# Kernel tuning notes

Measured on AMD Instinct MI355X. Metric: run time of the kernel, lower is better.

## Reference

```python
import jax, jax.numpy as jnp
import numpy as np
from jax.scipy.special import logsumexp

NUM_CLASSES = 2
THRESHOLD = 0.35      # overlap_thresh
NEGPOS_RATIO = 7      # neg_pos
VAR0, VAR1 = 0.1, 0.2  # self.variance


def point_form(p):
    # (cx,cy,w,h) -> (x1,y1,x2,y2)
    return jnp.concatenate([p[:, :2] - p[:, 2:] / 2, p[:, :2] + p[:, 2:] / 2], axis=1)


def jaccard(a, b):
    # a: [T,4] xyxy, b: [P,4] xyxy -> IoU [T,P]
    lt = jnp.maximum(a[:, None, :2], b[None, :, :2])
    rb = jnp.minimum(a[:, None, 2:], b[None, :, 2:])
    wh = jnp.clip(rb - lt, 0.0)
    inter = wh[..., 0] * wh[..., 1]
    area_a = ((a[:, 2] - a[:, 0]) * (a[:, 3] - a[:, 1]))[:, None]
    area_b = ((b[:, 2] - b[:, 0]) * (b[:, 3] - b[:, 1]))[None, :]
    return inter / (area_a + area_b - inter)


def encode(matched, priors):
    # matched xyxy [P,4], priors cxcywh [P,4]
    g_cxcy = ((matched[:, :2] + matched[:, 2:]) / 2 - priors[:, :2]) / (VAR0 * priors[:, 2:])
    g_wh = jnp.log((matched[:, 2:] - matched[:, :2]) / priors[:, 2:]) / VAR1
    return jnp.concatenate([g_cxcy, g_wh], axis=1)


def encode_landm(matched, priors):
    m = matched.reshape(-1, 5, 2)  # [P,5,2]
    g = (m - priors[:, None, :2]) / (VAR0 * priors[:, None, 2:])
    return g.reshape(-1, 10)


def match_one(truths, labels, landms, priors):
    # truths [T,4] xyxy, labels [T], landms [T,10], priors [P,4] cxcywh
    overlaps = jaccard(truths, point_form(priors))  # [T,P]
    best_prior_overlap = overlaps.max(axis=1)       # [T]
    best_prior_idx = overlaps.argmax(axis=1)        # [T]
    valid_gt = best_prior_overlap >= 0.2            # hard-gt filter
    best_truth_overlap = overlaps.max(axis=0)       # [P]
    best_truth_idx = overlaps.argmax(axis=0)        # [P]
    # index_fill_(0, best_prior_idx[valid], 2): IoU <= 1 so scatter-max is exact
    best_truth_overlap = best_truth_overlap.at[best_prior_idx].max(
        jnp.where(valid_gt, 2.0, 0.0))
    best_truth_idx = best_truth_idx.at[best_prior_idx].set(jnp.arange(truths.shape[0]))
    matches = truths[best_truth_idx]                # [P,4]
    conf = jnp.where(best_truth_overlap < THRESHOLD, 0.0, labels[best_truth_idx])
    loc = encode(matches, priors)
    landm = encode_landm(landms[best_truth_idx], priors)
    any_valid = valid_gt.any()                      # early-return branch in torch match()
    loc = jnp.where(any_valid, loc, 0.0)
    conf = jnp.where(any_valid, conf, 0.0)
    landm = jnp.where(any_valid, landm, 0.0)
    return loc, conf.astype(jnp.int32), landm


def smooth_l1(x):
    ax = jnp.abs(x)
    return jnp.where(ax < 1.0, 0.5 * ax * ax, ax - 0.5)


def multibox_loss(loc_data, conf_data, landm_data, priors, targets):
    num_priors = priors.shape[0]
    # torch uses .data (detached) for matching/encoding targets
    truths = jax.lax.stop_gradient(targets[..., :4])
    landms_gt = jax.lax.stop_gradient(targets[..., 4:14])
    labels = jax.lax.stop_gradient(targets[..., 14])
    pri = jax.lax.stop_gradient(priors)
    loc_t, conf_t, landm_t = jax.vmap(match_one, in_axes=(0, 0, 0, None))(
        truths, labels, landms_gt, pri)  # [B,P,4], [B,P], [B,P,10]

    # landmark loss over conf_t > 0
    pos1 = conf_t > 0
    N1 = jnp.maximum(pos1.sum().astype(jnp.float32), 1.0)
    loss_landm = jnp.sum(smooth_l1(landm_data - landm_t) * pos1[..., None])

    # localization loss over conf_t != 0; conf_t[pos] = 1
    pos = conf_t != 0
    conf_t = jnp.where(pos, 1, conf_t)
    loss_l = jnp.sum(smooth_l1(loc_data - loc_t) * pos[..., None])

    # per-prior CE = logsumexp(logits) - logit[target]
    ce = logsumexp(conf_data, axis=-1) - jnp.take_along_axis(
        conf_data, conf_t[..., None], axis=-1)[..., 0]  # [B,P]
    # hard negative mining: zero positives, double-argsort rank trick
    rank_loss = jnp.where(pos, 0.0, ce)
    idx_rank = jnp.argsort(jnp.argsort(-rank_loss, axis=1), axis=1)
    num_pos = pos.sum(axis=1, keepdims=True)
    num_neg = jnp.minimum(NEGPOS_RATIO * num_pos, num_priors - 1)
    neg = idx_rank < num_neg
    loss_c = jnp.sum(jnp.where(pos | neg, ce, 0.0))

    N = jnp.maximum(num_pos.sum().astype(jnp.float32), 1.0)
    return loss_l / N, loss_c / N, loss_landm / N1


def setup_inputs() -> dict:
    key = jax.random.key(0)
    ks = jax.random.split(key, 8)
    B, P, T = 16, 32768, 64
    loc_data = jax.random.normal(ks[0], (B, P, 4), jnp.float32)
    conf_data = jax.random.normal(ks[1], (B, P, NUM_CLASSES), jnp.float32)
    landm_data = jax.random.normal(ks[2], (B, P, 10), jnp.float32)
    # priors: (cx,cy,w,h), all positive and in (0,1)
    cxcy = jax.random.uniform(ks[3], (P, 2), minval=0.05, maxval=0.95)
    wh = jax.random.uniform(ks[4], (P, 2), minval=0.02, maxval=0.3)
    priors = jnp.concatenate([cxcy, wh], axis=1)
    # targets: [x1,y1,x2,y2, 10 landmark coords, label]
    c = jax.random.uniform(ks[5], (B, T, 2), minval=0.15, maxval=0.85)
    s = jax.random.uniform(ks[6], (B, T, 2), minval=0.05, maxval=0.25)
    boxes = jnp.concatenate([c - s / 2, c + s / 2], axis=-1)
    lm = jax.random.uniform(ks[7], (B, T, 10))
    labels = jnp.ones((B, T, 1), jnp.float32)
    targets = jnp.concatenate([boxes, lm, labels], axis=-1)
    return {"loc_data": loc_data, "conf_data": conf_data,
            "landm_data": landm_data, "priors": priors, "targets": targets}


def reference(loc_data, conf_data, landm_data, priors, targets):
    return multibox_loss(loc_data, conf_data, landm_data, priors, targets)
```

## Files before the change

kernel.cpp:

```cpp
#include <hip/hip_runtime.h>
#include <math.h>

#define OVERLAP_THRESH 0.35f
#define VALID_THRESH   0.2f
#define NEGPOS         7
#define TMAX           64
#define NCHUNK         16
#define TPW            4
#define EPT            4
#define HB             2048
#define NC             4
#define NSCAN          32

__device__ __forceinline__ float sl1(float x) {
    float ax = fabsf(x);
    return ax < 1.0f ? 0.5f * ax * ax : ax - 0.5f;
}
__device__ __forceinline__ float frcp(float x) { return __builtin_amdgcn_rcpf(x); }

__device__ __forceinline__ void atomicMaxU8(unsigned char* addr, unsigned char val) {
    size_t a = (size_t)addr;
    unsigned* word = (unsigned*)(a & ~(size_t)3);
    int shift = (int)(a & 3) * 8;
    unsigned old = *word, assumed;
    do {
        unsigned cur = (old >> shift) & 0xFFu;
        if (cur >= val) break;
        assumed = old;
        unsigned nw = (old & ~(0xFFu << shift)) | ((unsigned)val << shift);
        old = atomicCAS(word, assumed, nw);
    } while (old != assumed);
}

__global__ void clear_ws_kernel(uint4* __restrict__ p, size_t n16) {
    size_t i = (size_t)blockIdx.x * blockDim.x + threadIdx.x;
    size_t stride = (size_t)gridDim.x * blockDim.x;
    uint4 z = make_uint4(0u, 0u, 0u, 0u);
    for (; i < n16; i += stride) p[i] = z;
}

__device__ __forceinline__ void select_coarse(const int* gh, int K, int lane, int add0,
                                              int* s_d1, int* s_r) {
    int base = lane * 32;
    int v[32]; int s = 0;
    #pragma unroll
    for (int j = 0; j < 32; j++) {
        int h = gh[base + j];
        if (base + j == 0) h += add0;
        v[j] = h; s += h;
    }
    int sfx = s;
    for (int off = 1; off < 64; off <<= 1) {
        int t = __shfl_down(sfx, off);
        if (lane + off < 64) sfx += t;
    }
    int ge = sfx;
    #pragma unroll
    for (int j = 0; j < 32; j++) {
        int gen = ge - v[j];
        if (ge >= K && gen < K) { *s_d1 = base + j; *s_r = K - gen; }
        ge = gen;
    }
}

__global__ void best_prior_partial_kernel(const float* __restrict__ priors,
                                          const float* __restrict__ targets,
                                          int P, int BT,
                                          unsigned long long* __restrict__ keys) {
    int wid  = blockIdx.x * (blockDim.x >> 6) + (threadIdx.x >> 6);
    int lane = threadIdx.x & 63;
    int ng    = (BT + TPW - 1) / TPW;
    int group = wid % ng;
    int chunk = wid / ng;
    int bt0   = group * TPW;

    float tx1[TPW], ty1[TPW], tx2[TPW], ty2[TPW], ta[TPW];
    #pragma unroll
    for (int j = 0; j < TPW; j++) {
        int bt = min(bt0 + j, BT - 1);
        const float* tg = targets + (size_t)bt * 15;
        tx1[j] = tg[0]; ty1[j] = tg[1]; tx2[j] = tg[2]; ty2[j] = tg[3];
        ta[j]  = (tx2[j] - tx1[j]) * (ty2[j] - ty1[j]);
    }

    int cs = (P + NCHUNK - 1) / NCHUNK;
    int p0 = chunk * cs;
    int pend = min(p0 + cs, P);
    float best[TPW]; int bestp[TPW];
    #pragma unroll
    for (int j = 0; j < TPW; j++) { best[j] = -1.0f; bestp[j] = p0; }

    for (int p = p0 + lane; p < pend; p += 64) {
        float4 pr = ((const float4*)priors)[p];
        float hw = pr.z * 0.5f, hh = pr.w * 0.5f;
        float px1 = pr.x - hw, py1 = pr.y - hh;
        float px2 = pr.x + hw, py2 = pr.y + hh;
        float pa = (px2 - px1) * (py2 - py1);
        #pragma unroll
        for (int j = 0; j < TPW; j++) {
            float iw = fmaxf(fminf(tx2[j], px2) - fmaxf(tx1[j], px1), 0.0f);
            float ih = fmaxf(fminf(ty2[j], py2) - fmaxf(ty1[j], py1), 0.0f);
            float inter = iw * ih;
            float iou = inter * frcp(ta[j] + pa - inter);
            if (iou > best[j]) { best[j] = iou; bestp[j] = p; }
        }
    }
    #pragma unroll
    for (int j = 0; j < TPW; j++) {
        unsigned long long key =
            ((unsigned long long)__float_as_uint(fmaxf(best[j], 0.0f)) << 32) |
            (unsigned long long)(0xFFFFFFFFu - (unsigned)bestp[j]);
        for (int off = 32; off; off >>= 1) {
            unsigned long long k2 = __shfl_down(key, off);
            if (k2 > key) key = k2;
        }
        if (lane == 0 && bt0 + j < BT) atomicMax(&keys[bt0 + j], key);
    }
}

__global__ void unpack_override_kernel(const unsigned long long* __restrict__ keys,
                                       int T, int BT, int P,
                                       unsigned char* __restrict__ ovr8,
                                       unsigned* __restrict__ vmask,
                                       int* __restrict__ av_arr) {
    int i = blockIdx.x * blockDim.x + threadIdx.x;
    if (i >= BT) return;
    unsigned long long k = keys[i];
    int bpi = (int)(0xFFFFFFFFu - (unsigned)(k & 0xFFFFFFFFull));
    float iou = __uint_as_float((unsigned)(k >> 32));
    int b = i / T, t = i % T;
    atomicMaxU8(&ovr8[(size_t)b * P + bpi], (unsigned char)(t + 1));
    if (iou >= VALID_THRESH) {
        atomicOr(&vmask[(size_t)b * (P >> 5) + (bpi >> 5)], 1u << (bpi & 31));
        atomicOr(&av_arr[b], 1);
    }
}

__global__ void match_loss_fused_kernel(const float* __restrict__ priors,
                                        const float* __restrict__ targets,
                                        const float* __restrict__ loc_data,
                                        const float* __restrict__ conf_data,
                                        const float* __restrict__ landm_data,
                                        const unsigned char* __restrict__ ovr8,
                                        const unsigned* __restrict__ vmask,
                                        const int* __restrict__ av_arr,
                                        int P, int T,
                                        float* __restrict__ rank_loss,
                                        int* __restrict__ ghist,
                                        int* __restrict__ num_pos,
                                        int* __restrict__ num_pos1,
                                        float* __restrict__ accb)
{
    int b   = blockIdx.y;
    int tid = threadIdx.x;
    int p0  = (blockIdx.x * blockDim.x + tid) * EPT;
    size_t base = (size_t)b * P + p0;

    __shared__ float4 s_box[TMAX];
    __shared__ float  s_lab[TMAX];
    __shared__ int    s_hist[HB][NC];
    __shared__ float  s_ll, s_llm, s_cep;
    __shared__ int    s_np, s_np1;

    if (tid == 0) { s_ll = 0.f; s_llm = 0.f; s_cep = 0.f; s_np = 0; s_np1 = 0; }
    for (int i = tid; i < HB; i += blockDim.x)
        *(int4*)&s_hist[i][0] = make_int4(0, 0, 0, 0);
    if (tid < T) {
        const float* tg = targets + ((size_t)b * T + tid) * 15;
        s_box[tid] = make_float4(tg[0], tg[1], tg[2], tg[3]);
        s_lab[tid] = tg[14];
    }
    __syncthreads();

    int hc = tid & (NC - 1);
    int av = av_arr[b];
    float ll_s = 0.f, cep_s = 0.f, llm_s = 0.f;
    int np_s = 0, np1_s = 0;

    if (p0 + EPT <= P) {
        float px1[EPT], py1[EPT], px2[EPT], py2[EPT], pa[EPT];
        float pcx[EPT], pcy[EPT], pw[EPT], ph[EPT];
        float best[EPT]; int btidx[EPT];
        #pragma unroll
        for (int j = 0; j < EPT; j++) {
            float4 pr = ((const float4*)priors)[p0 + j];
            float hw = pr.z * 0.5f, hh = pr.w * 0.5f;
            px1[j] = pr.x - hw; py1[j] = pr.y - hh;
            px2[j] = pr.x + hw; py2[j] = pr.y + hh;
            pa[j]  = (px2[j] - px1[j]) * (py2[j] - py1[j]);
            pcx[j] = pr.x; pcy[j] = pr.y; pw[j] = pr.z; ph[j] = pr.w;
            best[j] = -1.0f; btidx[j] = 0;
        }

        const float* tg0 = targets + (size_t)b * T * 15;
        #pragma unroll 8
        for (int t = 0; t < TMAX; t++) {
            const float* tg = tg0 + t * 15;
            float bx1 = tg[0], by1 = tg[1], bx2 = tg[2], by2 = tg[3];
            float ba = (bx2 - bx1) * (by2 - by1);
            #pragma unroll
            for (int j = 0; j < EPT; j++) {
                float iw = fmaxf(fminf(bx2, px2[j]) - fmaxf(bx1, px1[j]), 0.0f);
                float ih = fmaxf(fminf(by2, py2[j]) - fmaxf(by1, py1[j]), 0.0f);
                float inter = iw * ih;
                float iou = inter * frcp(ba + pa[j] - inter);
                if (iou > best[j]) { best[j] = iou; btidx[j] = t; }
            }
        }

        unsigned ov4 = *(const unsigned*)&ovr8[base];
        unsigned vb  = vmask[(size_t)b * (P >> 5) + (p0 >> 5)] >> (p0 & 31);
        float cc[2 * EPT];
        *(float4*)&cc[0] = ((const float4*)(conf_data + base * 2))[0];
        *(float4*)&cc[4] = ((const float4*)(conf_data + base * 2))[1];

        float rl[EPT]; int btv[EPT]; float cev[EPT]; int posv[EPT];
        #pragma unroll
        for (int j = 0; j < EPT; j++) {
            int bt = btidx[j];
            int ov = (ov4 >> (8 * j)) & 0xFF;
            if (ov) bt = ov - 1;
            float bv = best[j];
            if ((vb >> j) & 1u) bv = 2.0f;
            btv[j] = bt;

            bool cond = (av && bv >= OVERLAP_THRESH);
            float lab = cond ? s_lab[bt] : 0.0f;
            int   ci  = (int)lab;
            bool  pos = cond && (ci != 0);
            posv[j] = pos;

            float c0 = cc[2 * j], c1 = cc[2 * j + 1];
            float mx = fmaxf(c0, c1);
            float lse = mx + __logf(1.0f + __expf(-fabsf(c0 - c1)));
            float ce  = lse - (pos ? c1 : c0);
            cev[j] = ce;
            rl[j] = pos ? 0.0f : fmaxf(ce, 0.0f);
            if (!pos) atomicAdd(&s_hist[__float_as_uint(rl[j]) >> 20][hc], 1);
        }
        *(float4*)&rank_loss[base] = *(float4*)rl;

        #pragma unroll
        for (int j = 0; j < EPT; j++) {
            if (!posv[j]) continue;
            int bt = btv[j];
            size_t idx = base + j;
            float4 mb = s_box[bt];
            bool pos1 = ((int)s_lab[bt] > 0);

            float rx = frcp(0.1f * pw[j]), ry = frcp(0.1f * ph[j]);
            float gx = ((mb.x + mb.z) * 0.5f - pcx[j]) * rx;
            float gy = ((mb.y + mb.w) * 0.5f - pcy[j]) * ry;
            float gw = __logf((mb.z - mb.x) * frcp(pw[j])) * 5.0f;
            float gh = __logf((mb.w - mb.y) * frcp(ph[j])) * 5.0f;
            const float* ld = loc_data + idx * 4;
            ll_s += sl1(ld[0] - gx) + sl1(ld[1] - gy) + sl1(ld[2] - gw) + sl1(ld[3] - gh);
            cep_s += cev[j];
            np_s++;

            if (pos1) {
                const float* lmd = landm_data + idx * 10;
                const float* lm  = targets + ((size_t)b * T + bt) * 15 + 4;
                float s = 0.0f;
                #pragma unroll
                for (int k = 0; k < 5; k++) {
                    float gxl = (lm[2 * k]     - pcx[j]) * rx;
                    float gyl = (lm[2 * k + 1] - pcy[j]) * ry;
                    s += sl1(lmd[2 * k] - gxl) + sl1(lmd[2 * k + 1] - gyl);
                }
                llm_s += s;
                np1_s++;
            }
        }
    }

    if (np_s)  { atomicAdd(&s_ll, ll_s); atomicAdd(&s_cep, cep_s); atomicAdd(&s_np, np_s); }
    if (np1_s) { atomicAdd(&s_llm, llm_s); atomicAdd(&s_np1, np1_s); }
    __syncthreads();
    if (tid == 0) {
        if (s_np)  { atomicAdd(&num_pos[b], s_np);
                     atomicAdd(&accb[b * 3 + 0], s_ll);
                     atomicAdd(&accb[b * 3 + 2], s_cep); }
        if (s_np1) { atomicAdd(&num_pos1[b], s_np1);
                     atomicAdd(&accb[b * 3 + 1], s_llm); }
    }
    for (int i = tid; i < HB; i += blockDim.x) {
        int4 v4 = *(int4*)&s_hist[i][0];
        int v = v4.x + v4.y + v4.z + v4.w;
        if (v) atomicAdd(&ghist[(size_t)b * HB + i], v);
    }
}

__device__ __forceinline__ void select_digit(const int* hist, int nb, int tid,
                                             int* s_dig, int* s_r) {
    if (tid < 64) {
        int lane = tid;
        int per  = (nb >= 64) ? (nb >> 6) : 1;
        int base = lane * per;
        int v[4]; int s = 0;
        #pragma unroll
        for (int j = 0; j < 4; j++) {
            int idx = base + j;
            int h = (j < per && idx < nb) ? hist[idx] : 0;
            v[j] = h; s += h;
        }
        int sfx = s;
        for (int off = 1; off < 64; off <<= 1) {
            int t = __shfl_down(sfx, off);
            if (lane + off < 64) sfx += t;
        }
        int r  = *s_r;
        int ge = sfx;
        #pragma unroll
        for (int j = 0; j < 4; j++) {
            int gen = ge - v[j];
            int d   = base + j;
            if (j < per && d < nb && ge >= r && gen < r) { *s_dig = d; *s_r = r - gen; }
            ge = gen;
        }
    }
}

__global__ void topk_scan_kernel(const float* __restrict__ rank_loss,
                                 const int* __restrict__ num_pos,
                                 const int* __restrict__ ghist,
                                 int P,
                                 float* __restrict__ glist,
                                 int* __restrict__ gcnt,
                                 float* __restrict__ accS,
                                 int* __restrict__ accC) {
    int b    = blockIdx.y;
    int tid  = threadIdx.x;
    int lane = tid & 63;
    int wv   = tid >> 6;
    int np   = num_pos[b];
    long long Kll = (long long)np * NEGPOS;
    int K = (Kll > P - 1) ? (P - 1) : (int)Kll;
    if (K <= 0) return;

    __shared__ int   s_d1, s_rdummy;
    __shared__ int   s_lcnt, s_base;
    __shared__ float s_stage[1024];
    __shared__ float s_S[4];
    __shared__ int   s_C[4];

    if (tid == 0) s_lcnt = 0;
    if (wv == 0) select_coarse(ghist + (size_t)b * HB, K, lane, np, &s_d1, &s_rdummy);
    __syncthreads();
    int d1 = s_d1;
    unsigned hi_lim = ((unsigned)(d1 + 1)) << 20;

    const float4* v4 = (const float4*)(rank_loss + (size_t)b * P);
    int n4  = P >> 2;
    int per = (n4 + NSCAN - 1) / NSCAN;
    int i0  = blockIdx.x * per;
    int i1  = min(i0 + per, n4);

    float S = 0.f; int C = 0;
    if (d1 == 0) {
        for (int i = i0 + tid; i < i1; i += blockDim.x) {
            float4 x = v4[i];
            float xs[4] = {x.x, x.y, x.z, x.w};
            #pragma unroll
            for (int k = 0; k < 4; k++) {
                unsigned u = __float_as_uint(xs[k]);
                if (u >= hi_lim) { S += xs[k]; C++; }
            }
        }
    } else {
        for (int i = i0 + tid; i < i1; i += blockDim.x) {
            float4 x = v4[i];
            float xs[4] = {x.x, x.y, x.z, x.w};
            #pragma unroll
            for (int k = 0; k < 4; k++) {
                unsigned u = __float_as_uint(xs[k]);
                if (u >= hi_lim) { S += xs[k]; C++; }
                bool m = ((u >> 20) == (unsigned)d1);
                unsigned long long mk = __ballot(m);
                if (m) {
                    int leader = __ffsll((long long)mk) - 1;
                    int base = 0;
                    if (lane == leader) base = atomicAdd(&s_lcnt, __popcll(mk));
                    base = __shfl(base, leader);
                    int ofs = __popcll(mk & (((unsigned long long)1 << lane) - 1ull));
                    s_stage[base + ofs] = xs[k];
                }
            }
        }
    }
    for (int off = 32; off; off >>= 1) {
        S += __shfl_down(S, off);
        C += __shfl_down(C, off);
    }
    if (lane == 0) { s_S[wv] = S; s_C[wv] = C; }
    __syncthreads();
    if (tid == 0) {
        float St = 0.f; int Ct = 0;
        for (int i = 0; i < 4; i++) { St += s_S[i]; Ct += s_C[i]; }
        if (Ct) { atomicAdd(&accS[b], St); atomicAdd(&accC[b], Ct); }
        s_base = s_lcnt ? atomicAdd(&gcnt[b], s_lcnt) : 0;
    }
    __syncthreads();
    int lc = s_lcnt, gbase = s_base;
    float* gl = glist + (size_t)b * P;
    for (int i = tid; i < lc; i += blockDim.x) gl[gbase + i] = s_stage[i];
}

__global__ void topk_refine_finalize_kernel(const int* __restrict__ num_pos,
                                            const int* __restrict__ num_pos1,
                                            const float* __restrict__ accb,
                                            const int* __restrict__ ghist,
                                            int P, int B,
                                            const float* __restrict__ glist,
                                            const int* __restrict__ gcnt,
                                            const float* __restrict__ accS,
                                            const int* __restrict__ accC,
                                            float* __restrict__ accn,
                                            int* __restrict__ done_ctr,
                                            float* __restrict__ out) {
    int b    = blockIdx.x;
    int tid  = threadIdx.x;
    int lane = tid & 63;
    int wv   = tid >> 6;
    int np   = num_pos[b];
    long long Kll = (long long)np * NEGPOS;
    int K = (Kll > P - 1) ? (P - 1) : (int)Kll;

    __shared__ int   hist[256];
    __shared__ int   s_d1, s_r, s_dig;
    __shared__ float s_S[16];
    __shared__ int   s_C[16];
    __shared__ float s_res;

    if (tid == 0) s_res = 0.0f;
    __syncthreads();

    if (K > 0) {
        if (wv == 0) select_coarse(ghist + (size_t)b * HB, K, lane, np, &s_d1, &s_r);
        __syncthreads();
        int d1 = s_d1;

        if (d1 == 0) {
            if (tid == 0) s_res = accS[b];
            __syncthreads();
        } else {
            int lc = gcnt[b];
            const float* gl = glist + (size_t)b * P;

            unsigned pmask = 0u, pval = 0u;
            const int shf[3] = {12, 4, 0};
            const int nbk[3] = {256, 256, 16};
            int trips = (lc + blockDim.x - 1) / blockDim.x;
            for (int ps = 0; ps < 3; ps++) {
                int sh = shf[ps]; unsigned wm = (unsigned)(nbk[ps] - 1);
                if (tid < 256) hist[tid] = 0;
                __syncthreads();
                for (int tc = 0; tc < trips; tc++) {
                    int i = tc * blockDim.x + tid;
                    bool ok = (i < lc);
                    unsigned u = ok ? __float_as_uint(gl[i]) : 0u;
                    ok = ok && ((u & pmask) == pval);
                    unsigned d = (u >> sh) & wm;
                    unsigned long long m = __ballot(ok);
                    #pragma unroll
                    for (int bit = 0; bit < 8; bit++) {
                        unsigned long long bb = __ballot((d >> bit) & 1u);
                        m &= ((d >> bit) & 1u) ? bb : ~bb;
                    }
                    if (ok && lane == (__ffsll((long long)m) - 1))
                        atomicAdd(&hist[d], __popcll(m));
                }
                __syncthreads();
                select_digit(hist, nbk[ps], tid, &s_dig, &s_r);
                __syncthreads();
                pval  |= ((unsigned)s_dig) << sh;
                pmask |= wm << sh;
            }
            float tau = __uint_as_float((((unsigned)d1) << 20) | pval);

            float S = 0.f; int C = 0;
            for (int i = tid; i < lc; i += blockDim.x) {
                float x = gl[i];
                if (x > tau) { S += x; C++; }
            }
            for (int off = 32; off; off >>= 1) {
                S += __shfl_down(S, off);
                C += __shfl_down(C, off);
            }
            if (lane == 0) { s_S[wv] = S; s_C[wv] = C; }
            __syncthreads();
            if (tid == 0) {
                float St = accS[b]; int Ct = accC[b];
                int nw = blockDim.x >> 6;
                for (int i = 0; i < nw; i++) { St += s_S[i]; Ct += s_C[i]; }
                s_res = St + (float)(K - Ct) * tau;
            }
            __syncthreads();
        }
    }

    if (tid == 0) {
        accn[b] = s_res;
        __threadfence();
        if (atomicAdd(done_ctr, 1) == B - 1) {
            float cen = 0.f;
            for (int j = 0; j < B; j++) cen += atomicAdd(&accn[j], 0.0f);
            int tp = 0, tp1 = 0;
            float ll = 0.f, llm = 0.f, cep = 0.f;
            for (int j = 0; j < B; j++) {
                tp  += num_pos[j];
                tp1 += num_pos1[j];
                ll  += accb[j * 3 + 0];
                llm += accb[j * 3 + 1];
                cep += accb[j * 3 + 2];
            }
            float N  = fmaxf((float)tp, 1.0f);
            float N1 = fmaxf((float)tp1, 1.0f);
            out[0] = ll / N;
            out[1] = (cep + cen) / N;
            out[2] = llm / N1;
        }
    }
}

extern "C" void kernel_launch(void* const* d_in, const int* in_sizes, int n_in,
                              void* d_out, int out_size, void* d_ws, size_t ws_size,
                              hipStream_t stream) {
    const float* loc_data   = (const float*)d_in[0];
    const float* conf_data  = (const float*)d_in[1];
    const float* landm_data = (const float*)d_in[2];
    const float* priors     = (const float*)d_in[3];
    const float* targets    = (const float*)d_in[4];
    float* out = (float*)d_out;

    int P  = in_sizes[3] / 4;
    int BP = in_sizes[0] / 4;
    int B  = BP / P;
    int T  = in_sizes[4] / (B * 15);
    int BT = B * T;

    char* ws = (char*)d_ws;
    float* rank_loss = (float*)ws;                    size_t off = (size_t)B * P * sizeof(float);
    float* glist     = (float*)(ws + off);            off += (size_t)B * P * sizeof(float);
    unsigned char* ovr8 = (unsigned char*)(ws + off); off += (size_t)B * P;
    unsigned* vmask = (unsigned*)(ws + off); off += (size_t)B * (P >> 5) * sizeof(unsigned);
    int* ghist      = (int*)(ws + off);      off += (size_t)B * HB * sizeof(int);
    unsigned long long* keys = (unsigned long long*)(ws + off); off += (size_t)BT * sizeof(unsigned long long);
    int* av_arr     = (int*)(ws + off);      off += (size_t)B * sizeof(int);
    int* num_pos    = (int*)(ws + off);      off += (size_t)B * sizeof(int);
    int* num_pos1   = (int*)(ws + off);      off += (size_t)B * sizeof(int);
    float* accb     = (float*)(ws + off);    off += (size_t)B * 3 * sizeof(float);
    float* accn     = (float*)(ws + off);    off += (size_t)B * sizeof(float);
    int* gcnt       = (int*)(ws + off);      off += (size_t)B * sizeof(int);
    float* accS     = (float*)(ws + off);    off += (size_t)B * sizeof(float);
    int* accC       = (int*)(ws + off);      off += (size_t)B * sizeof(int);
    int* done_ctr   = (int*)(ws + off);      off += sizeof(int);

    size_t zbytes = (size_t)((char*)(done_ctr + 1) - (char*)ovr8);
    size_t n16 = (zbytes + 15) / 16;
    clear_ws_kernel<<<256, 256, 0, stream>>>((uint4*)ovr8, n16);

    int waves   = NCHUNK * ((BT + TPW - 1) / TPW);
    int blocks2 = (waves + 3) / 4;
    best_prior_partial_kernel<<<blocks2, 256, 0, stream>>>(priors, targets, P, BT, keys);

    unpack_override_kernel<<<(BT + 255) / 256, 256, 0, stream>>>(keys, T, BT, P,
                                                                 ovr8, vmask, av_arr);

    dim3 gm((P + 256 * EPT - 1) / (256 * EPT), B);
    match_loss_fused_kernel<<<gm, 256, 0, stream>>>(priors, targets, loc_data, conf_data,
                                                    landm_data, ovr8, vmask, av_arr, P, T,
                                                    rank_loss, ghist, num_pos, num_pos1, accb);

    dim3 gs(NSCAN, B);
    topk_scan_kernel<<<gs, 256, 0, stream>>>(rank_loss, num_pos, ghist, P,
                                             glist, gcnt, accS, accC);

    topk_refine_finalize_kernel<<<B, 1024, 0, stream>>>(num_pos, num_pos1, accb, ghist,
                                                        P, B, glist, gcnt, accS, accC,
                                                        accn, done_ctr, out);
}
```

Baseline: 106.3 us.

## Fuse override unpack into best-prior kernel and compare IoU by cross-multiplication

Removes the separate unpack_override kernel launch. The last-finishing wave per target group, detected with a per-group done counter and threadfences, now writes the override byte, valid mask and any-valid flag. Both IoU argmax loops also stop calling a reciprocal per pair. They compare inter*best_union against best_inter*union and compute a single reciprocal at the end. This saves one launch and a per-pair rcp, but adds atomics and fences at the end of each wave, and the cross-multiplied comparison can break ties slightly differently from the rcp-based one.

```diff
diff --git a/kernel.cpp b/kernel.cpp
--- a/kernel.cpp
+++ b/kernel.cpp
@@ -65,8 +65,12 @@
 
 __global__ void best_prior_partial_kernel(const float* __restrict__ priors,
                                           const float* __restrict__ targets,
-                                          int P, int BT,
-                                          unsigned long long* __restrict__ keys) {
+                                          int P, int T, int BT,
+                                          unsigned long long* __restrict__ keys,
+                                          int* __restrict__ done_grp,
+                                          unsigned char* __restrict__ ovr8,
+                                          unsigned* __restrict__ vmask,
+                                          int* __restrict__ av_arr) {
     int wid  = blockIdx.x * (blockDim.x >> 6) + (threadIdx.x >> 6);
     int lane = threadIdx.x & 63;
     int ng    = (BT + TPW - 1) / TPW;
@@ -86,9 +90,9 @@
     int cs = (P + NCHUNK - 1) / NCHUNK;
     int p0 = chunk * cs;
     int pend = min(p0 + cs, P);
-    float best[TPW]; int bestp[TPW];
+    float bi[TPW], bu[TPW]; int bestp[TPW];
     #pragma unroll
-    for (int j = 0; j < TPW; j++) { best[j] = -1.0f; bestp[j] = p0; }
+    for (int j = 0; j < TPW; j++) { bi[j] = -1.0f; bu[j] = 1.0f; bestp[j] = p0; }
 
     for (int p = p0 + lane; p < pend; p += 64) {
         float4 pr = ((const float4*)priors)[p];
@@ -101,14 +105,17 @@
             float iw = fmaxf(fminf(tx2[j], px2) - fmaxf(tx1[j], px1), 0.0f);
             float ih = fmaxf(fminf(ty2[j], py2) - fmaxf(ty1[j], py1), 0.0f);
             float inter = iw * ih;
-            float iou = inter * frcp(ta[j] + pa - inter);
-            if (iou > best[j]) { best[j] = iou; bestp[j] = p; }
+            float uni = ta[j] + pa - inter;
+            if (inter * bu[j] > bi[j] * uni) {
+                bi[j] = inter; bu[j] = uni; bestp[j] = p;
+            }
         }
     }
     #pragma unroll
     for (int j = 0; j < TPW; j++) {
+        float iou = bi[j] * frcp(bu[j]);
         unsigned long long key =
-            ((unsigned long long)__float_as_uint(fmaxf(best[j], 0.0f)) << 32) |
+            ((unsigned long long)__float_as_uint(fmaxf(iou, 0.0f)) << 32) |
             (unsigned long long)(0xFFFFFFFFu - (unsigned)bestp[j]);
         for (int off = 32; off; off >>= 1) {
             unsigned long long k2 = __shfl_down(key, off);
@@ -116,23 +123,25 @@
         }
         if (lane == 0 && bt0 + j < BT) atomicMax(&keys[bt0 + j], key);
     }
-}
-
-__global__ void unpack_override_kernel(const unsigned long long* __restrict__ keys,
-                                       int T, int BT, int P,
-                                       unsigned char* __restrict__ ovr8,
-                                       unsigned* __restrict__ vmask,
-                                       int* __restrict__ av_arr) {
-    int i = blockIdx.x * blockDim.x + threadIdx.x;
-    if (i >= BT) return;
-    unsigned long long k = keys[i];
-    int bpi = (int)(0xFFFFFFFFu - (unsigned)(k & 0xFFFFFFFFull));
-    float iou = __uint_as_float((unsigned)(k >> 32));
-    int b = i / T, t = i % T;
-    atomicMaxU8(&ovr8[(size_t)b * P + bpi], (unsigned char)(t + 1));
-    if (iou >= VALID_THRESH) {
-        atomicOr(&vmask[(size_t)b * (P >> 5) + (bpi >> 5)], 1u << (bpi & 31));
-        atomicOr(&av_arr[b], 1);
+
+    if (lane == 0) {
+        __threadfence();
+        if (atomicAdd(&done_grp[group], 1) == NCHUNK - 1) {
+            __threadfence();
+            for (int j = 0; j < TPW; j++) {
+                int bt = bt0 + j;
+                if (bt >= BT) break;
+                unsigned long long k = atomicAdd(&keys[bt], 0ull);
+                int bpi = (int)(0xFFFFFFFFu - (unsigned)(k & 0xFFFFFFFFull));
+                float iou = __uint_as_float((unsigned)(k >> 32));
+                int b = bt / T, t = bt % T;
+                atomicMaxU8(&ovr8[(size_t)b * P + bpi], (unsigned char)(t + 1));
+                if (iou >= VALID_THRESH) {
+                    atomicOr(&vmask[(size_t)b * (P >> 5) + (bpi >> 5)], 1u << (bpi & 31));
+                    atomicOr(&av_arr[b], 1);
+                }
+            }
+        }
     }
 }
 
@@ -180,7 +189,7 @@
     if (p0 + EPT <= P) {
         float px1[EPT], py1[EPT], px2[EPT], py2[EPT], pa[EPT];
         float pcx[EPT], pcy[EPT], pw[EPT], ph[EPT];
-        float best[EPT]; int btidx[EPT];
+        float bi[EPT], bu[EPT]; int btidx[EPT];
         #pragma unroll
         for (int j = 0; j < EPT; j++) {
             float4 pr = ((const float4*)priors)[p0 + j];
@@ -189,7 +198,7 @@
             px2[j] = pr.x + hw; py2[j] = pr.y + hh;
             pa[j]  = (px2[j] - px1[j]) * (py2[j] - py1[j]);
             pcx[j] = pr.x; pcy[j] = pr.y; pw[j] = pr.z; ph[j] = pr.w;
-            best[j] = -1.0f; btidx[j] = 0;
+            bi[j] = -1.0f; bu[j] = 1.0f; btidx[j] = 0;
         }
 
         const float* tg0 = targets + (size_t)b * T * 15;
@@ -203,8 +212,10 @@
                 float iw = fmaxf(fminf(bx2, px2[j]) - fmaxf(bx1, px1[j]), 0.0f);
                 float ih = fmaxf(fminf(by2, py2[j]) - fmaxf(by1, py1[j]), 0.0f);
                 float inter = iw * ih;
-                float iou = inter * frcp(ba + pa[j] - inter);
-                if (iou > best[j]) { best[j] = iou; btidx[j] = t; }
+                float uni = ba + pa[j] - inter;
+                if (inter * bu[j] > bi[j] * uni) {
+                    bi[j] = inter; bu[j] = uni; btidx[j] = t;
+                }
             }
         }
 
@@ -220,7 +231,7 @@
             int bt = btidx[j];
             int ov = (ov4 >> (8 * j)) & 0xFF;
             if (ov) bt = ov - 1;
-            float bv = best[j];
+            float bv = bi[j] * frcp(bu[j]);
             if ((vb >> j) & 1u) bv = 2.0f;
             btv[j] = bt;
 
@@ -538,6 +549,7 @@
     int B  = BP / P;
     int T  = in_sizes[4] / (B * 15);
     int BT = B * T;
+    int ng = (BT + TPW - 1) / TPW;
 
     char* ws = (char*)d_ws;
     float* rank_loss = (float*)ws;                    size_t off = (size_t)B * P * sizeof(float);
@@ -546,6 +558,7 @@
     unsigned* vmask = (unsigned*)(ws + off); off += (size_t)B * (P >> 5) * sizeof(unsigned);
     int* ghist      = (int*)(ws + off);      off += (size_t)B * HB * sizeof(int);
     unsigned long long* keys = (unsigned long long*)(ws + off); off += (size_t)BT * sizeof(unsigned long long);
+    int* done_grp   = (int*)(ws + off);      off += (size_t)ng * sizeof(int);
     int* av_arr     = (int*)(ws + off);      off += (size_t)B * sizeof(int);
     int* num_pos    = (int*)(ws + off);      off += (size_t)B * sizeof(int);
     int* num_pos1   = (int*)(ws + off);      off += (size_t)B * sizeof(int);
@@ -560,12 +573,11 @@
     size_t n16 = (zbytes + 15) / 16;
     clear_ws_kernel<<<256, 256, 0, stream>>>((uint4*)ovr8, n16);
 
-    int waves   = NCHUNK * ((BT + TPW - 1) / TPW);
+    int waves   = NCHUNK * ng;
     int blocks2 = (waves + 3) / 4;
-    best_prior_partial_kernel<<<blocks2, 256, 0, stream>>>(priors, targets, P, BT, keys);
-
-    unpack_override_kernel<<<(BT + 255) / 256, 256, 0, stream>>>(keys, T, BT, P,
-                                                                 ovr8, vmask, av_arr);
+    best_prior_partial_kernel<<<blocks2, 256, 0, stream>>>(priors, targets, P, T, BT,
+                                                           keys, done_grp,
+                                                           ovr8, vmask, av_arr);
 
     dim3 gm((P + 256 * EPT - 1) / (256 * EPT), B);
     match_loss_fused_kernel<<<gm, 256, 0, stream>>>(priors, targets, loc_data, conf_data,
```

After: 160.2 us. 1.51x slower.
